# Kernel tuning notes

Hardware: AMD Instinct MI355X
Metric: run time of the kernel (lower is better)

Reference implementation:

```python
import jax, jax.numpy as jnp
import numpy as np

NEG = -1e9

def setup_inputs() -> dict:
    key = jax.random.key(0)
    k1, k2, k3, k4, k5 = jax.random.split(key, 5)
    B, S, D = 4, 2048, 1024
    x = jax.random.normal(k1, (B, S, D), dtype=jnp.float32)
    Wq = jax.random.normal(k2, (D, D), dtype=jnp.float32) * (1.0 / np.sqrt(D))
    Wk = jax.random.normal(k3, (D, D), dtype=jnp.float32) * (1.0 / np.sqrt(D))
    Wv = jax.random.normal(k4, (D, D), dtype=jnp.float32) * (1.0 / np.sqrt(D))
    mask = jax.random.randint(k5, (B, S), 0, 2) > 0  # bool [B,S]
    return {"x": x, "Wq": Wq, "Wk": Wk, "Wv": Wv, "mask": mask}

def reference(x, Wq, Wk, Wv, mask):
    # x: [B,S,D]; single-head self-attention, scale = 1/sqrt(D)
    D = x.shape[-1]
    scale = 1.0 / D ** 0.5
    q = jnp.einsum('bsi,ij->bsj', x, Wq)
    k = jnp.einsum('bsi,ij->bsj', x, Wk)
    y = jnp.einsum('bsi,bzi->bsz', q, k) * scale  # [B,S,S]
    # additive mask: (~mask)[:, :, None] * -1e9 broadcasts over key axis
    m = (~mask).astype(jnp.float32)[:, :, None]
    y = y + m * NEG
    v = jnp.einsum('bsi,ij->bsj', x, Wv)
    attn = jax.nn.softmax(y, axis=-1)
    return jnp.einsum('bsz,bzi->bsi', attn, v)
```

## Files before the change

kernel.cpp:

```cpp
#include <hip/hip_runtime.h>

typedef __bf16 bf16x8 __attribute__((ext_vector_type(8)));
typedef float f32x4 __attribute__((ext_vector_type(4)));
typedef unsigned short u16;

__device__ __forceinline__ u16 f2bf(float f) {
    union { float f; unsigned u; } v; v.f = f;
    unsigned r = (v.u + 0x7FFFu + ((v.u >> 16) & 1u)) >> 16;
    return (u16)r;
}

__device__ __forceinline__ void fence_bar() {
    asm volatile("" ::: "memory");
    __builtin_amdgcn_s_barrier();
    asm volatile("" ::: "memory");
}

__global__ __launch_bounds__(256)
void normMask(const unsigned int* __restrict__ m, unsigned char* __restrict__ nm) {
    __shared__ int isByte;
    if (threadIdx.x == 0) isByte = 0;
    __syncthreads();
    int bad = 0;
    for (int i = threadIdx.x; i < 2048; i += 256) bad |= (m[i] > 1u);
    if (bad) atomicOr(&isByte, 1);
    __syncthreads();
    if (isByte) {
        const unsigned char* mb = (const unsigned char*)m;
        for (int i = threadIdx.x; i < 8192; i += 256) nm[i] = mb[i] ? 1 : 0;
    } else {
        for (int i = threadIdx.x; i < 8192; i += 256) nm[i] = (unsigned char)m[i];
    }
}

__global__ __launch_bounds__(256)
void transW(const float* __restrict__ Wq, const float* __restrict__ Wk,
            const float* __restrict__ Wv, u16* __restrict__ Wt) {
    __shared__ u16 tile[64][65];
    const float* W = blockIdx.z == 0 ? Wq : (blockIdx.z == 1 ? Wk : Wv);
    u16* out = Wt + (size_t)blockIdx.z * 1024 * 1024;
    int k0 = blockIdx.x * 64, n0 = blockIdx.y * 64;
    int t = threadIdx.x, cl = t & 63, rw = t >> 6;
    #pragma unroll
    for (int r = 0; r < 16; ++r) {
        int row = r * 4 + rw;
        tile[cl][row] = f2bf(W[(size_t)(k0 + row) * 1024 + n0 + cl]);
    }
    __syncthreads();
    #pragma unroll
    for (int r = 0; r < 16; ++r) {
        int row = r * 4 + rw;
        out[(size_t)(n0 + row) * 1024 + k0 + cl] = tile[row][cl];
    }
}

__global__ __launch_bounds__(256)
void convX(const float* __restrict__ x, u16* __restrict__ xb) {
    const size_t n4 = (size_t)8192 * 1024 / 4;
    for (size_t i = (size_t)blockIdx.x * 256 + threadIdx.x; i < n4; i += (size_t)gridDim.x * 256) {
        float4 v = ((const float4*)x)[i];
        ushort4 o = make_ushort4(f2bf(v.x), f2bf(v.y), f2bf(v.z), f2bf(v.w));
        ((ushort4*)xb)[i] = o;
    }
}

__global__ __launch_bounds__(256)
void transV(const u16* __restrict__ qkv, u16* __restrict__ vt) {
    __shared__ u16 tile[64][65];
    int b = blockIdx.z;
    int s0 = blockIdx.x * 64, d0 = blockIdx.y * 64;
    int t = threadIdx.x, cl = t & 63, rw = t >> 6;
    const u16* src = qkv + (size_t)b * 2048 * 3072 + 2048;
    #pragma unroll
    for (int r = 0; r < 16; ++r) {
        int row = r * 4 + rw;
        tile[cl][row] = src[(size_t)(s0 + row) * 3072 + d0 + cl];
    }
    __syncthreads();
    u16* dst = vt + (size_t)b * 1024 * 2048;
    #pragma unroll
    for (int r = 0; r < 16; ++r) {
        int row = r * 4 + rw;
        dst[(size_t)(d0 + row) * 2048 + s0 + cl] = tile[row][cl];
    }
}

template <int OUTV>
__global__ __launch_bounds__(512, 2)
void gemm8p(const u16* __restrict__ A_, int lda, size_t sA,
            const u16* __restrict__ B_, int ldb, size_t sB,
            void* __restrict__ Cout, int ldc, size_t sC,
            int kdim, int ntiles) {
    __shared__ u16 lds[65536];
    const u16* A = A_ + (size_t)blockIdx.z * sA;
    const u16* B = B_ + (size_t)blockIdx.z * sB;

    const int bid = blockIdx.x;
    const int brow = (bid / ntiles) * 256, bcol = (bid % ntiles) * 256;
    const int t = threadIdx.x;
    const int w = t >> 6, l = t & 63;
    const int wr = w >> 2, wc = w & 3;

    const int srow = t >> 3;
    const int sslot = (t & 7) ^ (srow & 7);
    const int aBase = (wr * 128 + (l & 15)) * 64;
    const int bBase = 32768 + (wc * 64 + (l & 15)) * 64;
    const int cx0 = (((l >> 4)) ^ (l & 7)) * 8;
    const int cx1 = (((l >> 4) + 4) ^ (l & 7)) * 8;

    auto lds3 = (__attribute__((address_space(3))) char*)lds;

    #define ISSUE(matB, q, tt, buf) do {                                           \
        const u16* gsrc = ((matB) ? B : A)                                         \
            + (size_t)(((matB) ? bcol : brow) + (q) * 64 + srow) * ((matB) ? ldb : lda) \
            + (size_t)(tt) * 64 + sslot * 8;                                       \
        const int dst_ = ((matB) ? 32768 : 0) + (buf) * 16384 + (q) * 4096 + t * 8; \
        __builtin_amdgcn_global_load_lds(                                          \
            (const __attribute__((address_space(1))) void*)gsrc,                   \
            (__attribute__((address_space(3))) void*)(lds3 + 2 * dst_), 16, 0, 0); \
    } while (0)

    f32x4 acc[8][4];
    #pragma unroll
    for (int m = 0; m < 8; ++m)
        #pragma unroll
        for (int n = 0; n < 4; ++n)
            acc[m][n] = (f32x4){0.f, 0.f, 0.f, 0.f};

    const int NT = kdim >> 6;

    ISSUE(1, 0, 0, 0); ISSUE(1, 1, 0, 0); ISSUE(1, 2, 0, 0); ISSUE(1, 3, 0, 0);
    ISSUE(0, 0, 0, 0); ISSUE(0, 2, 0, 0); ISSUE(0, 1, 0, 0); ISSUE(0, 3, 0, 0);
    asm volatile("s_waitcnt vmcnt(2)" ::: "memory");
    fence_bar();

    for (int tt = 0; tt < NT; ++tt) {
        const int c = tt & 1;
        const int ab = c * 16384;
        const int nb = c ^ 1;
        const bool pf = (tt + 1 < NT);
        bf16x8 af[4], bfv[4];

        #pragma unroll
        for (int m = 0; m < 4; ++m) af[m] = *(const bf16x8*)&lds[ab + aBase + m * 1024 + cx0];
        #pragma unroll
        for (int n = 0; n < 4; ++n) bfv[n] = *(const bf16x8*)&lds[ab + bBase + n * 1024 + cx0];
        if (pf) {
            ISSUE(1, 0, tt + 1, nb); ISSUE(1, 1, tt + 1, nb);
            asm volatile("s_waitcnt vmcnt(2)" ::: "memory");
        } else {
            asm volatile("s_waitcnt vmcnt(0)" ::: "memory");
        }
        fence_bar();
        __builtin_amdgcn_s_setprio(1);
        #pragma unroll
        for (int m = 0; m < 4; ++m)
            #pragma unroll
            for (int n = 0; n < 4; ++n)
                acc[m][n] = __builtin_amdgcn_mfma_f32_16x16x32_bf16(af[m], bfv[n], acc[m][n], 0, 0, 0);
        __builtin_amdgcn_s_setprio(0);
        fence_bar();

        #pragma unroll
        for (int m = 0; m < 4; ++m) af[m] = *(const bf16x8*)&lds[ab + aBase + (m + 4) * 1024 + cx0];
        if (pf) { ISSUE(1, 2, tt + 1, nb); ISSUE(1, 3, tt + 1, nb); }
        fence_bar();
        __builtin_amdgcn_s_setprio(1);
        #pragma unroll
        for (int m = 0; m < 4; ++m)
            #pragma unroll
            for (int n = 0; n < 4; ++n)
                acc[m + 4][n] = __builtin_amdgcn_mfma_f32_16x16x32_bf16(af[m], bfv[n], acc[m + 4][n], 0, 0, 0);
        __builtin_amdgcn_s_setprio(0);
        fence_bar();

        #pragma unroll
        for (int m = 0; m < 4; ++m) af[m] = *(const bf16x8*)&lds[ab + aBase + m * 1024 + cx1];
        #pragma unroll
        for (int n = 0; n < 4; ++n) bfv[n] = *(const bf16x8*)&lds[ab + bBase + n * 1024 + cx1];
        if (pf) { ISSUE(0, 0, tt + 1, nb); ISSUE(0, 2, tt + 1, nb); }
        fence_bar();
        __builtin_amdgcn_s_setprio(1);
        #pragma unroll
        for (int m = 0; m < 4; ++m)
            #pragma unroll
            for (int n = 0; n < 4; ++n)
                acc[m][n] = __builtin_amdgcn_mfma_f32_16x16x32_bf16(af[m], bfv[n], acc[m][n], 0, 0, 0);
        __builtin_amdgcn_s_setprio(0);
        fence_bar();

        #pragma unroll
        for (int m = 0; m < 4; ++m) af[m] = *(const bf16x8*)&lds[ab + aBase + (m + 4) * 1024 + cx1];
        if (pf) {
            ISSUE(0, 1, tt + 1, nb); ISSUE(0, 3, tt + 1, nb);
            asm volatile("s_waitcnt vmcnt(2)" ::: "memory");
        } else {
            asm volatile("s_waitcnt vmcnt(0)" ::: "memory");
        }
        fence_bar();
        __builtin_amdgcn_s_setprio(1);
        #pragma unroll
        for (int m = 0; m < 4; ++m)
            #pragma unroll
            for (int n = 0; n < 4; ++n)
                acc[m + 4][n] = __builtin_amdgcn_mfma_f32_16x16x32_bf16(af[m], bfv[n], acc[m + 4][n], 0, 0, 0);
        __builtin_amdgcn_s_setprio(0);
        fence_bar();
    }
    #undef ISSUE

    const int lr = (l >> 4) * 4, lc = l & 15;
    #pragma unroll
    for (int m = 0; m < 8; ++m) {
        #pragma unroll
        for (int n = 0; n < 4; ++n) {
            int rr = brow + wr * 128 + m * 16 + lr;
            int cc = bcol + wc * 64 + n * 16 + lc;
            #pragma unroll
            for (int j = 0; j < 4; ++j) {
                if constexpr (OUTV == 0)
                    ((u16*)Cout)[(size_t)blockIdx.z * sC + (size_t)(rr + j) * ldc + cc] = f2bf(acc[m][n][j]);
                else
                    ((float*)Cout)[(size_t)blockIdx.z * sC + (size_t)(rr + j) * ldc + cc] = acc[m][n][j];
            }
        }
    }
}

template <int OUTV>
__global__ __launch_bounds__(256, 2)
void gemm_bt(const u16* __restrict__ A0, int lda, size_t sA,
             const u16* __restrict__ B0, int ldb, size_t sB,
             void* __restrict__ Cout, int ldc, size_t sC, int kdim) {
    __shared__ u16 lA[128 * 64];
    __shared__ u16 lB[128 * 64];
    const u16* A = A0 + (size_t)blockIdx.z * sA;
    const u16* B = B0 + (size_t)blockIdx.z * sB;
    const int t = threadIdx.x;
    const int w = t >> 6, l = t & 63;
    const int wr = w >> 1, wc = w & 1;
    const int brow = blockIdx.x * 128, bcol = blockIdx.y * 128;
    const int rt = l >> 3;
    const int cb = (l & 7) * 8;

    auto ldsA3 = (__attribute__((address_space(3))) char*)lA;
    auto ldsB3 = (__attribute__((address_space(3))) char*)lB;

    f32x4 acc[4][4];
    #pragma unroll
    for (int m = 0; m < 4; ++m)
        #pragma unroll
        for (int n = 0; n < 4; ++n)
            acc[m][n] = (f32x4){0.f, 0.f, 0.f, 0.f};

    for (int k0 = 0; k0 < kdim; k0 += 64) {
        __syncthreads();
        #pragma unroll
        for (int p = 0; p < 4; ++p) {
            int chunk = p * 4 + w;
            const u16* ga = A + (size_t)(brow + chunk * 8 + rt) * lda + k0 + cb;
            __builtin_amdgcn_global_load_lds(
                (const __attribute__((address_space(1))) void*)ga,
                (__attribute__((address_space(3))) void*)(ldsA3 + chunk * 1024), 16, 0, 0);
            const u16* gb = B + (size_t)(bcol + chunk * 8 + rt) * ldb + k0 + cb;
            __builtin_amdgcn_global_load_lds(
                (const __attribute__((address_space(1))) void*)gb,
                (__attribute__((address_space(3))) void*)(ldsB3 + chunk * 1024), 16, 0, 0);
        }
        __syncthreads();
        #pragma unroll
        for (int kk = 0; kk < 2; ++kk) {
            bf16x8 af[4], bfv[4];
            #pragma unroll
            for (int m = 0; m < 4; ++m)
                af[m] = *(const bf16x8*)&lA[(wr * 64 + m * 16 + (l & 15)) * 64 + kk * 32 + (l >> 4) * 8];
            #pragma unroll
            for (int n = 0; n < 4; ++n)
                bfv[n] = *(const bf16x8*)&lB[(wc * 64 + n * 16 + (l & 15)) * 64 + kk * 32 + (l >> 4) * 8];
            #pragma unroll
            for (int m = 0; m < 4; ++m)
                #pragma unroll
                for (int n = 0; n < 4; ++n)
                    acc[m][n] = __builtin_amdgcn_mfma_f32_16x16x32_bf16(af[m], bfv[n], acc[m][n], 0, 0, 0);
        }
    }

    const int lrow = (l >> 4) * 4, lcol = l & 15;
    #pragma unroll
    for (int m = 0; m < 4; ++m) {
        #pragma unroll
        for (int n = 0; n < 4; ++n) {
            int rr = brow + wr * 64 + m * 16 + lrow;
            int cc = bcol + wc * 64 + n * 16 + lcol;
            #pragma unroll
            for (int j = 0; j < 4; ++j) {
                if constexpr (OUTV == 0)
                    ((u16*)Cout)[(size_t)blockIdx.z * sC + (size_t)(rr + j) * ldc + cc] = f2bf(acc[m][n][j]);
                else
                    ((float*)Cout)[(size_t)blockIdx.z * sC + (size_t)(rr + j) * ldc + cc] = acc[m][n][j];
            }
        }
    }
}

__global__ __launch_bounds__(256)
void softmax_rows(const float* __restrict__ S0, size_t sS, u16* __restrict__ P0, size_t sP,
                  const unsigned char* __restrict__ nm, int bbase) {
    const int row = blockIdx.x, t = threadIdx.x;
    const int b = bbase + blockIdx.z;
    const float* S = S0 + (size_t)blockIdx.z * sS;
    u16* dst = P0 + (size_t)blockIdx.z * sP + (size_t)row * 2048;
    if (nm[b * 2048 + row] == 0) {
        ushort4 u = make_ushort4(0x3A00, 0x3A00, 0x3A00, 0x3A00);
        ((ushort4*)dst)[t] = u;
        ((ushort4*)dst)[t + 256] = u;
        return;
    }
    const float4* src = (const float4*)(S + (size_t)row * 2048);
    float4 a = src[t], c = src[t + 256];
    float v[8] = {a.x, a.y, a.z, a.w, c.x, c.y, c.z, c.w};
    float mx = -1e30f;
    #pragma unroll
    for (int i = 0; i < 8; ++i) { v[i] *= 0.03125f; mx = fmaxf(mx, v[i]); }
    #pragma unroll
    for (int o = 32; o > 0; o >>= 1) mx = fmaxf(mx, __shfl_xor(mx, o));
    __shared__ float redm[4], reds[4];
    if ((t & 63) == 0) redm[t >> 6] = mx;
    __syncthreads();
    mx = fmaxf(fmaxf(redm[0], redm[1]), fmaxf(redm[2], redm[3]));
    float s = 0.f;
    #pragma unroll
    for (int i = 0; i < 8; ++i) { v[i] = expf(v[i] - mx); s += v[i]; }
    #pragma unroll
    for (int o = 32; o > 0; o >>= 1) s += __shfl_xor(s, o);
    if ((t & 63) == 0) reds[t >> 6] = s;
    __syncthreads();
    s = (reds[0] + reds[1]) + (reds[2] + reds[3]);
    float inv = 1.0f / s;
    ushort4 o0 = make_ushort4(f2bf(v[0] * inv), f2bf(v[1] * inv), f2bf(v[2] * inv), f2bf(v[3] * inv));
    ushort4 o1 = make_ushort4(f2bf(v[4] * inv), f2bf(v[5] * inv), f2bf(v[6] * inv), f2bf(v[7] * inv));
    ((ushort4*)dst)[t] = o0;
    ((ushort4*)dst)[t + 256] = o1;
}

extern "C" void kernel_launch(void* const* d_in, const int* in_sizes, int n_in,
                              void* d_out, int out_size, void* d_ws, size_t ws_size,
                              hipStream_t stream) {
    const float* x  = (const float*)d_in[0];
    const float* Wq = (const float*)d_in[1];
    const float* Wk = (const float*)d_in[2];
    const float* Wv = (const float*)d_in[3];
    const unsigned int* mask = (const unsigned int*)d_in[4];
    float* out = (float*)d_out;

    char* p = (char*)d_ws;
    u16* Wt  = (u16*)p;  p += (size_t)3072 * 1024 * 2;
    u16* xb  = (u16*)p;  p += (size_t)8192 * 1024 * 2;
    u16* qkv = (u16*)p;  p += (size_t)8192 * 3072 * 2;
    u16* vt  = (u16*)p;  p += (size_t)4 * 1024 * 2048 * 2;
    char* base = p;
    const size_t sizeS = (size_t)2048 * 2048 * 4;
    const size_t sizeP = (size_t)2048 * 2048 * 2;
    bool batched = ws_size >= (size_t)(base - (char*)d_ws) + 4 * (sizeS + sizeP) + 8192;

    float* S = (float*)base;
    u16* P;
    unsigned char* nm;
    if (batched) {
        P  = (u16*)(base + 4 * sizeS);
        nm = (unsigned char*)(base + 4 * (sizeS + sizeP));
    } else {
        P  = (u16*)(base + sizeS);
        nm = (unsigned char*)(base + sizeS + sizeP);
    }

    normMask<<<1, 256, 0, stream>>>(mask, nm);
    transW<<<dim3(16, 16, 3), 256, 0, stream>>>(Wq, Wk, Wv, Wt);
    convX<<<2048, 256, 0, stream>>>(x, xb);
    gemm8p<0><<<dim3(384, 1, 1), 512, 0, stream>>>(
        xb, 1024, 0, Wt, 1024, 0, qkv, 3072, 0, 1024, 12);
    transV<<<dim3(32, 16, 4), 256, 0, stream>>>(qkv, vt);

    if (batched) {
        gemm8p<1><<<dim3(64, 1, 4), 512, 0, stream>>>(
            qkv, 3072, (size_t)2048 * 3072, qkv + 1024, 3072, (size_t)2048 * 3072,
            S, 2048, (size_t)2048 * 2048, 1024, 8);
        softmax_rows<<<dim3(2048, 1, 4), 256, 0, stream>>>(
            S, (size_t)2048 * 2048, P, (size_t)2048 * 2048, nm, 0);
        gemm_bt<2><<<dim3(16, 8, 4), 256, 0, stream>>>(
            P, 2048, (size_t)2048 * 2048, vt, 2048, (size_t)1024 * 2048,
            out, 1024, (size_t)2048 * 1024, 2048);
    } else {
        for (int b = 0; b < 4; ++b) {
            const u16* Qb = qkv + (size_t)b * 2048 * 3072;
            gemm8p<1><<<dim3(64, 1, 1), 512, 0, stream>>>(
                Qb, 3072, 0, Qb + 1024, 3072, 0, S, 2048, 0, 1024, 8);
            softmax_rows<<<dim3(2048, 1, 1), 256, 0, stream>>>(S, 0, P, 0, nm, b);
            gemm_bt<2><<<dim3(16, 8, 1), 256, 0, stream>>>(
                P, 2048, 0, vt + (size_t)b * 1024 * 2048, 2048, 0,
                out + (size_t)b * 2048 * 1024, 1024, 0, 2048);
        }
    }
}
```

Before: 201.3 us.

## Add XCD-aware block swizzle and issue whole next-tile prefetch at once

Adds a template flag that remaps block IDs so that consecutive tiles, which share A/B panels, land on the same XCD, aiming for better L2 reuse in the QKV projection and the batched QK^T GEMM. It also restructures the K-loop prefetch: instead of spreading the eight next-tile async loads across four compute stages, it waits for all outstanding loads and then issues all eight at the start of each iteration. The swizzle assumes the grid size divides by 8. The bulk prefetch trades finer-grained overlap for an earlier issue, and adds a full vmcnt(0) stall at the top of every iteration.

New measurement: 205.5 us. 2.1% more time.

```diff
diff --git a/kernel.cpp b/kernel.cpp
--- a/kernel.cpp
+++ b/kernel.cpp
@@ -85,7 +85,7 @@
     }
 }
 
-template <int OUTV>
+template <int OUTV, int SWZ>
 __global__ __launch_bounds__(512, 2)
 void gemm8p(const u16* __restrict__ A_, int lda, size_t sA,
             const u16* __restrict__ B_, int ldb, size_t sB,
@@ -95,7 +95,11 @@
     const u16* A = A_ + (size_t)blockIdx.z * sA;
     const u16* B = B_ + (size_t)blockIdx.z * sB;
 
-    const int bid = blockIdx.x;
+    int bid = blockIdx.x;
+    if (SWZ) {
+        int cpx = gridDim.x >> 3;
+        bid = (bid & 7) * cpx + (bid >> 3);
+    }
     const int brow = (bid / ntiles) * 256, bcol = (bid % ntiles) * 256;
     const int t = threadIdx.x;
     const int w = t >> 6, l = t & 63;
@@ -120,6 +124,13 @@
             (__attribute__((address_space(3))) void*)(lds3 + 2 * dst_), 16, 0, 0); \
     } while (0)
 
+    #define ISSUE8(tt, buf) do {                                                   \
+        ISSUE(1, 0, tt, buf); ISSUE(1, 1, tt, buf);                                \
+        ISSUE(1, 2, tt, buf); ISSUE(1, 3, tt, buf);                                \
+        ISSUE(0, 0, tt, buf); ISSUE(0, 2, tt, buf);                                \
+        ISSUE(0, 1, tt, buf); ISSUE(0, 3, tt, buf);                                \
+    } while (0)
+
     f32x4 acc[8][4];
     #pragma unroll
     for (int m = 0; m < 8; ++m)
@@ -129,9 +140,8 @@
 
     const int NT = kdim >> 6;
 
-    ISSUE(1, 0, 0, 0); ISSUE(1, 1, 0, 0); ISSUE(1, 2, 0, 0); ISSUE(1, 3, 0, 0);
-    ISSUE(0, 0, 0, 0); ISSUE(0, 2, 0, 0); ISSUE(0, 1, 0, 0); ISSUE(0, 3, 0, 0);
-    asm volatile("s_waitcnt vmcnt(2)" ::: "memory");
+    ISSUE8(0, 0);
+    asm volatile("s_waitcnt vmcnt(0)" ::: "memory");
     fence_bar();
 
     for (int tt = 0; tt < NT; ++tt) {
@@ -145,12 +155,8 @@
         for (int m = 0; m < 4; ++m) af[m] = *(const bf16x8*)&lds[ab + aBase + m * 1024 + cx0];
         #pragma unroll
         for (int n = 0; n < 4; ++n) bfv[n] = *(const bf16x8*)&lds[ab + bBase + n * 1024 + cx0];
-        if (pf) {
-            ISSUE(1, 0, tt + 1, nb); ISSUE(1, 1, tt + 1, nb);
-            asm volatile("s_waitcnt vmcnt(2)" ::: "memory");
-        } else {
-            asm volatile("s_waitcnt vmcnt(0)" ::: "memory");
-        }
+        asm volatile("s_waitcnt vmcnt(0)" ::: "memory");
+        if (pf) ISSUE8(tt + 1, nb);
         fence_bar();
         __builtin_amdgcn_s_setprio(1);
         #pragma unroll
@@ -163,7 +169,6 @@
 
         #pragma unroll
         for (int m = 0; m < 4; ++m) af[m] = *(const bf16x8*)&lds[ab + aBase + (m + 4) * 1024 + cx0];
-        if (pf) { ISSUE(1, 2, tt + 1, nb); ISSUE(1, 3, tt + 1, nb); }
         fence_bar();
         __builtin_amdgcn_s_setprio(1);
         #pragma unroll
@@ -178,7 +183,6 @@
         for (int m = 0; m < 4; ++m) af[m] = *(const bf16x8*)&lds[ab + aBase + m * 1024 + cx1];
         #pragma unroll
         for (int n = 0; n < 4; ++n) bfv[n] = *(const bf16x8*)&lds[ab + bBase + n * 1024 + cx1];
-        if (pf) { ISSUE(0, 0, tt + 1, nb); ISSUE(0, 2, tt + 1, nb); }
         fence_bar();
         __builtin_amdgcn_s_setprio(1);
         #pragma unroll
@@ -191,12 +195,8 @@
 
         #pragma unroll
         for (int m = 0; m < 4; ++m) af[m] = *(const bf16x8*)&lds[ab + aBase + (m + 4) * 1024 + cx1];
-        if (pf) {
-            ISSUE(0, 1, tt + 1, nb); ISSUE(0, 3, tt + 1, nb);
-            asm volatile("s_waitcnt vmcnt(2)" ::: "memory");
-        } else {
-            asm volatile("s_waitcnt vmcnt(0)" ::: "memory");
-        }
+        if (pf) asm volatile("s_waitcnt vmcnt(2)" ::: "memory");
+        else    asm volatile("s_waitcnt vmcnt(0)" ::: "memory");
         fence_bar();
         __builtin_amdgcn_s_setprio(1);
         #pragma unroll
@@ -207,6 +207,7 @@
         __builtin_amdgcn_s_setprio(0);
         fence_bar();
     }
+    #undef ISSUE8
     #undef ISSUE
 
     const int lr = (l >> 4) * 4, lc = l & 15;
@@ -377,12 +378,12 @@
     normMask<<<1, 256, 0, stream>>>(mask, nm);
     transW<<<dim3(16, 16, 3), 256, 0, stream>>>(Wq, Wk, Wv, Wt);
     convX<<<2048, 256, 0, stream>>>(x, xb);
-    gemm8p<0><<<dim3(384, 1, 1), 512, 0, stream>>>(
+    gemm8p<0, 1><<<dim3(384, 1, 1), 512, 0, stream>>>(
         xb, 1024, 0, Wt, 1024, 0, qkv, 3072, 0, 1024, 12);
     transV<<<dim3(32, 16, 4), 256, 0, stream>>>(qkv, vt);
 
     if (batched) {
-        gemm8p<1><<<dim3(64, 1, 4), 512, 0, stream>>>(
+        gemm8p<1, 1><<<dim3(64, 1, 4), 512, 0, stream>>>(
             qkv, 3072, (size_t)2048 * 3072, qkv + 1024, 3072, (size_t)2048 * 3072,
             S, 2048, (size_t)2048 * 2048, 1024, 8);
         softmax_rows<<<dim3(2048, 1, 4), 256, 0, stream>>>(
@@ -393,7 +394,7 @@
     } else {
         for (int b = 0; b < 4; ++b) {
             const u16* Qb = qkv + (size_t)b * 2048 * 3072;
-            gemm8p<1><<<dim3(64, 1, 1), 512, 0, stream>>>(
+            gemm8p<1, 0><<<dim3(64, 1, 1), 512, 0, stream>>>(
                 Qb, 3072, 0, Qb + 1024, 3072, 0, S, 2048, 0, 1024, 8);
             softmax_rows<<<dim3(2048, 1, 1), 256, 0, stream>>>(S, 0, P, 0, nm, b);
             gemm_bt<2><<<dim3(16, 8, 1), 256, 0, stream>>>(
```

## Fuse softmax into QK epilogue stats and PV GEMM prologue

Applied to the files above, without the earlier changes.

Drops the separate softmax kernel and the bf16 P matrix. The QK^T GEMM epilogue now writes per-row partial max and sum-exp for each 64-column slice, a small kernel combines these into a row max and inverse sum, and the PV GEMM recomputes exp from the fp32 scores as it loads them into shared memory. The 1/sqrt(D) scale is folded into Wq during its bf16 conversion, and masked rows are encoded as a negative inverse-sum sentinel that yields a uniform 1/2048. The aim is to skip one full read of S and a write plus read of P, at the cost of exp work and register-path fp32 loads inside the PV GEMM's load loop in place of async global-to-LDS copies.

After: 256.6 us. 27.5% more time.

```diff
diff --git a/kernel.cpp b/kernel.cpp
--- a/kernel.cpp
+++ b/kernel.cpp
@@ -38,13 +38,14 @@
             const float* __restrict__ Wv, u16* __restrict__ Wt) {
     __shared__ u16 tile[64][65];
     const float* W = blockIdx.z == 0 ? Wq : (blockIdx.z == 1 ? Wk : Wv);
+    const float sc = blockIdx.z == 0 ? 0.03125f : 1.0f;
     u16* out = Wt + (size_t)blockIdx.z * 1024 * 1024;
     int k0 = blockIdx.x * 64, n0 = blockIdx.y * 64;
     int t = threadIdx.x, cl = t & 63, rw = t >> 6;
     #pragma unroll
     for (int r = 0; r < 16; ++r) {
         int row = r * 4 + rw;
-        tile[cl][row] = f2bf(W[(size_t)(k0 + row) * 1024 + n0 + cl]);
+        tile[cl][row] = f2bf(W[(size_t)(k0 + row) * 1024 + n0 + cl] * sc);
     }
     __syncthreads();
     #pragma unroll
@@ -90,7 +91,7 @@
 void gemm8p(const u16* __restrict__ A_, int lda, size_t sA,
             const u16* __restrict__ B_, int ldb, size_t sB,
             void* __restrict__ Cout, int ldc, size_t sC,
-            int kdim, int ntiles) {
+            int kdim, int ntiles, float2* __restrict__ partPtr) {
     __shared__ u16 lds[65536];
     const u16* A = A_ + (size_t)blockIdx.z * sA;
     const u16* B = B_ + (size_t)blockIdx.z * sB;
@@ -225,16 +226,61 @@
             }
         }
     }
-}
-
-template <int OUTV>
+    if constexpr (OUTV == 1) {
+        float2* part = partPtr + ((size_t)blockIdx.z * 32 + (bcol >> 6) + wc) * 2048;
+        #pragma unroll
+        for (int m = 0; m < 8; ++m) {
+            #pragma unroll
+            for (int j = 0; j < 4; ++j) {
+                float mx = fmaxf(fmaxf(acc[m][0][j], acc[m][1][j]),
+                                 fmaxf(acc[m][2][j], acc[m][3][j]));
+                #pragma unroll
+                for (int o = 1; o < 16; o <<= 1) mx = fmaxf(mx, __shfl_xor(mx, o));
+                float se = 0.f;
+                #pragma unroll
+                for (int n = 0; n < 4; ++n) se += __expf(acc[m][n][j] - mx);
+                #pragma unroll
+                for (int o = 1; o < 16; o <<= 1) se += __shfl_xor(se, o);
+                if ((l & 15) == 0) {
+                    int rr = brow + wr * 128 + m * 16 + (l >> 4) * 4 + j;
+                    part[rr] = make_float2(mx, se);
+                }
+            }
+        }
+    }
+}
+
+__global__ __launch_bounds__(256)
+void combineStats(const float2* __restrict__ part, float2* __restrict__ stats,
+                  const unsigned char* __restrict__ nm, int bbase) {
+    const int row = blockIdx.x * 256 + threadIdx.x;
+    const int z = blockIdx.y;
+    if (nm[(bbase + z) * 2048 + row] == 0) {
+        stats[z * 2048 + row] = make_float2(0.f, -(1.0f / 2048.0f));
+        return;
+    }
+    const float2* p = part + (size_t)z * 32 * 2048 + row;
+    float m = -1e30f;
+    #pragma unroll
+    for (int c = 0; c < 32; ++c) m = fmaxf(m, p[(size_t)c * 2048].x);
+    float Z = 0.f;
+    #pragma unroll
+    for (int c = 0; c < 32; ++c) {
+        float2 v = p[(size_t)c * 2048];
+        Z += v.y * __expf(v.x - m);
+    }
+    stats[z * 2048 + row] = make_float2(m, 1.0f / Z);
+}
+
 __global__ __launch_bounds__(256, 2)
-void gemm_bt(const u16* __restrict__ A0, int lda, size_t sA,
+void gemm_pv(const float* __restrict__ S0, size_t sS,
+             const float2* __restrict__ st0,
              const u16* __restrict__ B0, int ldb, size_t sB,
-             void* __restrict__ Cout, int ldc, size_t sC, int kdim) {
+             float* __restrict__ Cout, int ldc, size_t sC, int kdim) {
     __shared__ u16 lA[128 * 64];
     __shared__ u16 lB[128 * 64];
-    const u16* A = A0 + (size_t)blockIdx.z * sA;
+    const float* S = S0 + (size_t)blockIdx.z * sS;
+    const float2* st = st0 + (size_t)blockIdx.z * 2048;
     const u16* B = B0 + (size_t)blockIdx.z * sB;
     const int t = threadIdx.x;
     const int w = t >> 6, l = t & 63;
@@ -243,8 +289,14 @@
     const int rt = l >> 3;
     const int cb = (l & 7) * 8;
 
-    auto ldsA3 = (__attribute__((address_space(3))) char*)lA;
     auto ldsB3 = (__attribute__((address_space(3))) char*)lB;
+
+    float sm[4], siz[4];
+    #pragma unroll
+    for (int p = 0; p < 4; ++p) {
+        float2 v = st[brow + (p * 4 + w) * 8 + rt];
+        sm[p] = v.x; siz[p] = v.y;
+    }
 
     f32x4 acc[4][4];
     #pragma unroll
@@ -258,14 +310,22 @@
         #pragma unroll
         for (int p = 0; p < 4; ++p) {
             int chunk = p * 4 + w;
-            const u16* ga = A + (size_t)(brow + chunk * 8 + rt) * lda + k0 + cb;
-            __builtin_amdgcn_global_load_lds(
-                (const __attribute__((address_space(1))) void*)ga,
-                (__attribute__((address_space(3))) void*)(ldsA3 + chunk * 1024), 16, 0, 0);
             const u16* gb = B + (size_t)(bcol + chunk * 8 + rt) * ldb + k0 + cb;
             __builtin_amdgcn_global_load_lds(
                 (const __attribute__((address_space(1))) void*)gb,
                 (__attribute__((address_space(3))) void*)(ldsB3 + chunk * 1024), 16, 0, 0);
+            const float4* sp = (const float4*)(S + (size_t)(brow + chunk * 8 + rt) * 2048 + k0 + cb);
+            float4 a0 = sp[0], a1 = sp[1];
+            float m = sm[p], iz = siz[p];
+            float pv[8] = {a0.x, a0.y, a0.z, a0.w, a1.x, a1.y, a1.z, a1.w};
+            unsigned ou[4];
+            #pragma unroll
+            for (int i = 0; i < 4; ++i) {
+                float p0 = iz < 0.f ? -iz : __expf(pv[2 * i]     - m) * iz;
+                float p1 = iz < 0.f ? -iz : __expf(pv[2 * i + 1] - m) * iz;
+                ou[i] = (unsigned)f2bf(p0) | ((unsigned)f2bf(p1) << 16);
+            }
+            *(uint4*)&lA[chunk * 512 + l * 8] = make_uint4(ou[0], ou[1], ou[2], ou[3]);
         }
         __syncthreads();
         #pragma unroll
@@ -293,54 +353,10 @@
             int rr = brow + wr * 64 + m * 16 + lrow;
             int cc = bcol + wc * 64 + n * 16 + lcol;
             #pragma unroll
-            for (int j = 0; j < 4; ++j) {
-                if constexpr (OUTV == 0)
-                    ((u16*)Cout)[(size_t)blockIdx.z * sC + (size_t)(rr + j) * ldc + cc] = f2bf(acc[m][n][j]);
-                else
-                    ((float*)Cout)[(size_t)blockIdx.z * sC + (size_t)(rr + j) * ldc + cc] = acc[m][n][j];
-            }
-        }
-    }
-}
-
-__global__ __launch_bounds__(256)
-void softmax_rows(const float* __restrict__ S0, size_t sS, u16* __restrict__ P0, size_t sP,
-                  const unsigned char* __restrict__ nm, int bbase) {
-    const int row = blockIdx.x, t = threadIdx.x;
-    const int b = bbase + blockIdx.z;
-    const float* S = S0 + (size_t)blockIdx.z * sS;
-    u16* dst = P0 + (size_t)blockIdx.z * sP + (size_t)row * 2048;
-    if (nm[b * 2048 + row] == 0) {
-        ushort4 u = make_ushort4(0x3A00, 0x3A00, 0x3A00, 0x3A00);
-        ((ushort4*)dst)[t] = u;
-        ((ushort4*)dst)[t + 256] = u;
-        return;
-    }
-    const float4* src = (const float4*)(S + (size_t)row * 2048);
-    float4 a = src[t], c = src[t + 256];
-    float v[8] = {a.x, a.y, a.z, a.w, c.x, c.y, c.z, c.w};
-    float mx = -1e30f;
-    #pragma unroll
-    for (int i = 0; i < 8; ++i) { v[i] *= 0.03125f; mx = fmaxf(mx, v[i]); }
-    #pragma unroll
-    for (int o = 32; o > 0; o >>= 1) mx = fmaxf(mx, __shfl_xor(mx, o));
-    __shared__ float redm[4], reds[4];
-    if ((t & 63) == 0) redm[t >> 6] = mx;
-    __syncthreads();
-    mx = fmaxf(fmaxf(redm[0], redm[1]), fmaxf(redm[2], redm[3]));
-    float s = 0.f;
-    #pragma unroll
-    for (int i = 0; i < 8; ++i) { v[i] = expf(v[i] - mx); s += v[i]; }
-    #pragma unroll
-    for (int o = 32; o > 0; o >>= 1) s += __shfl_xor(s, o);
-    if ((t & 63) == 0) reds[t >> 6] = s;
-    __syncthreads();
-    s = (reds[0] + reds[1]) + (reds[2] + reds[3]);
-    float inv = 1.0f / s;
-    ushort4 o0 = make_ushort4(f2bf(v[0] * inv), f2bf(v[1] * inv), f2bf(v[2] * inv), f2bf(v[3] * inv));
-    ushort4 o1 = make_ushort4(f2bf(v[4] * inv), f2bf(v[5] * inv), f2bf(v[6] * inv), f2bf(v[7] * inv));
-    ((ushort4*)dst)[t] = o0;
-    ((ushort4*)dst)[t + 256] = o1;
+            for (int j = 0; j < 4; ++j)
+                Cout[(size_t)blockIdx.z * sC + (size_t)(rr + j) * ldc + cc] = acc[m][n][j];
+        }
+    }
 }
 
 extern "C" void kernel_launch(void* const* d_in, const int* in_sizes, int n_in,
@@ -359,45 +375,41 @@
     u16* qkv = (u16*)p;  p += (size_t)8192 * 3072 * 2;
     u16* vt  = (u16*)p;  p += (size_t)4 * 1024 * 2048 * 2;
     char* base = p;
-    const size_t sizeS = (size_t)2048 * 2048 * 4;
-    const size_t sizeP = (size_t)2048 * 2048 * 2;
-    bool batched = ws_size >= (size_t)(base - (char*)d_ws) + 4 * (sizeS + sizeP) + 8192;
-
-    float* S = (float*)base;
-    u16* P;
-    unsigned char* nm;
-    if (batched) {
-        P  = (u16*)(base + 4 * sizeS);
-        nm = (unsigned char*)(base + 4 * (sizeS + sizeP));
-    } else {
-        P  = (u16*)(base + sizeS);
-        nm = (unsigned char*)(base + sizeS + sizeP);
-    }
+    const size_t sizeS  = (size_t)2048 * 2048 * 4;
+    const size_t sizePt = (size_t)32 * 2048 * 8;
+    const size_t sizeSt = (size_t)2048 * 8;
+    bool batched = ws_size >= (size_t)(base - (char*)d_ws) + 4 * (sizeS + sizePt + sizeSt) + 8192;
+
+    float* S; float2* part; float2* stats; unsigned char* nm;
+    int nz = batched ? 4 : 1;
+    S     = (float*)base;
+    part  = (float2*)(base + nz * sizeS);
+    stats = (float2*)(base + nz * (sizeS + sizePt));
+    nm    = (unsigned char*)(base + nz * (sizeS + sizePt + sizeSt));
 
     normMask<<<1, 256, 0, stream>>>(mask, nm);
     transW<<<dim3(16, 16, 3), 256, 0, stream>>>(Wq, Wk, Wv, Wt);
     convX<<<2048, 256, 0, stream>>>(x, xb);
     gemm8p<0><<<dim3(384, 1, 1), 512, 0, stream>>>(
-        xb, 1024, 0, Wt, 1024, 0, qkv, 3072, 0, 1024, 12);
+        xb, 1024, 0, Wt, 1024, 0, qkv, 3072, 0, 1024, 12, nullptr);
     transV<<<dim3(32, 16, 4), 256, 0, stream>>>(qkv, vt);
 
     if (batched) {
         gemm8p<1><<<dim3(64, 1, 4), 512, 0, stream>>>(
             qkv, 3072, (size_t)2048 * 3072, qkv + 1024, 3072, (size_t)2048 * 3072,
-            S, 2048, (size_t)2048 * 2048, 1024, 8);
-        softmax_rows<<<dim3(2048, 1, 4), 256, 0, stream>>>(
-            S, (size_t)2048 * 2048, P, (size_t)2048 * 2048, nm, 0);
-        gemm_bt<2><<<dim3(16, 8, 4), 256, 0, stream>>>(
-            P, 2048, (size_t)2048 * 2048, vt, 2048, (size_t)1024 * 2048,
+            S, 2048, (size_t)2048 * 2048, 1024, 8, part);
+        combineStats<<<dim3(8, 4), 256, 0, stream>>>(part, stats, nm, 0);
+        gemm_pv<<<dim3(16, 8, 4), 256, 0, stream>>>(
+            S, (size_t)2048 * 2048, stats, vt, 2048, (size_t)1024 * 2048,
             out, 1024, (size_t)2048 * 1024, 2048);
     } else {
         for (int b = 0; b < 4; ++b) {
             const u16* Qb = qkv + (size_t)b * 2048 * 3072;
             gemm8p<1><<<dim3(64, 1, 1), 512, 0, stream>>>(
-                Qb, 3072, 0, Qb + 1024, 3072, 0, S, 2048, 0, 1024, 8);
-            softmax_rows<<<dim3(2048, 1, 1), 256, 0, stream>>>(S, 0, P, 0, nm, b);
-            gemm_bt<2><<<dim3(16, 8, 1), 256, 0, stream>>>(
-                P, 2048, 0, vt + (size_t)b * 1024 * 2048, 2048, 0,
+                Qb, 3072, 0, Qb + 1024, 3072, 0, S, 2048, 0, 1024, 8, part);
+            combineStats<<<dim3(8, 1), 256, 0, stream>>>(part, stats, nm, b);
+            gemm_pv<<<dim3(16, 8, 1), 256, 0, stream>>>(
+                S, 0, stats, vt + (size_t)b * 1024 * 2048, 2048, 0,
                 out + (size_t)b * 2048 * 1024, 1024, 0, 2048);
         }
     }
```

## Replace LDS-staged attention GEMMs with register-direct global loads and double buffering

Applied to the files above, without the earlier changes.

Swaps the LDS-staged gemm_bt and the persistent gemm8p for the QK^T and PV products with a new gemm_reg kernel. Each lane loads its MFMA fragments straight from global memory into registers, double-buffered over 32-wide k steps, with no shared memory and no barriers. This drops LDS traffic and sync overhead but gives up reuse across waves, so each tile is reloaded from global/L2 several times and more memory bandwidth is needed. The occupancy hint of 2 in launch_bounds is also removed.

After: 343.6 us (median of 4 runs). +70.7%, slower.

```diff
diff --git a/kernel.cpp b/kernel.cpp
--- a/kernel.cpp
+++ b/kernel.cpp
@@ -228,23 +228,25 @@
 }
 
 template <int OUTV>
-__global__ __launch_bounds__(256, 2)
-void gemm_bt(const u16* __restrict__ A0, int lda, size_t sA,
-             const u16* __restrict__ B0, int ldb, size_t sB,
-             void* __restrict__ Cout, int ldc, size_t sC, int kdim) {
-    __shared__ u16 lA[128 * 64];
-    __shared__ u16 lB[128 * 64];
+__global__ __launch_bounds__(256)
+void gemm_reg(const u16* __restrict__ A0, int lda, size_t sA,
+              const u16* __restrict__ B0, int ldb, size_t sB,
+              float* __restrict__ Cout, int ldc, size_t sC, int kdim) {
     const u16* A = A0 + (size_t)blockIdx.z * sA;
     const u16* B = B0 + (size_t)blockIdx.z * sB;
     const int t = threadIdx.x;
     const int w = t >> 6, l = t & 63;
     const int wr = w >> 1, wc = w & 1;
     const int brow = blockIdx.x * 128, bcol = blockIdx.y * 128;
-    const int rt = l >> 3;
-    const int cb = (l & 7) * 8;
-
-    auto ldsA3 = (__attribute__((address_space(3))) char*)lA;
-    auto ldsB3 = (__attribute__((address_space(3))) char*)lB;
+
+    const u16* pA[4];
+    const u16* pB[4];
+    #pragma unroll
+    for (int m = 0; m < 4; ++m)
+        pA[m] = A + (size_t)(brow + wr * 64 + m * 16 + (l & 15)) * lda + (l >> 4) * 8;
+    #pragma unroll
+    for (int n = 0; n < 4; ++n)
+        pB[n] = B + (size_t)(bcol + wc * 64 + n * 16 + (l & 15)) * ldb + (l >> 4) * 8;
 
     f32x4 acc[4][4];
     #pragma unroll
@@ -253,37 +255,34 @@
         for (int n = 0; n < 4; ++n)
             acc[m][n] = (f32x4){0.f, 0.f, 0.f, 0.f};
 
-    for (int k0 = 0; k0 < kdim; k0 += 64) {
-        __syncthreads();
-        #pragma unroll
-        for (int p = 0; p < 4; ++p) {
-            int chunk = p * 4 + w;
-            const u16* ga = A + (size_t)(brow + chunk * 8 + rt) * lda + k0 + cb;
-            __builtin_amdgcn_global_load_lds(
-                (const __attribute__((address_space(1))) void*)ga,
-                (__attribute__((address_space(3))) void*)(ldsA3 + chunk * 1024), 16, 0, 0);
-            const u16* gb = B + (size_t)(bcol + chunk * 8 + rt) * ldb + k0 + cb;
-            __builtin_amdgcn_global_load_lds(
-                (const __attribute__((address_space(1))) void*)gb,
-                (__attribute__((address_space(3))) void*)(ldsB3 + chunk * 1024), 16, 0, 0);
-        }
-        __syncthreads();
-        #pragma unroll
-        for (int kk = 0; kk < 2; ++kk) {
-            bf16x8 af[4], bfv[4];
-            #pragma unroll
-            for (int m = 0; m < 4; ++m)
-                af[m] = *(const bf16x8*)&lA[(wr * 64 + m * 16 + (l & 15)) * 64 + kk * 32 + (l >> 4) * 8];
-            #pragma unroll
-            for (int n = 0; n < 4; ++n)
-                bfv[n] = *(const bf16x8*)&lB[(wc * 64 + n * 16 + (l & 15)) * 64 + kk * 32 + (l >> 4) * 8];
-            #pragma unroll
-            for (int m = 0; m < 4; ++m)
-                #pragma unroll
-                for (int n = 0; n < 4; ++n)
-                    acc[m][n] = __builtin_amdgcn_mfma_f32_16x16x32_bf16(af[m], bfv[n], acc[m][n], 0, 0, 0);
-        }
-    }
+    #define LOADH(aa, bb, h) do {                                        \
+        const int ko = (h) * 32;                                         \
+        _Pragma("unroll")                                                \
+        for (int m = 0; m < 4; ++m) aa[m] = *(const bf16x8*)(pA[m] + ko);\
+        _Pragma("unroll")                                                \
+        for (int n = 0; n < 4; ++n) bb[n] = *(const bf16x8*)(pB[n] + ko);\
+    } while (0)
+
+    #define MFMA16(aa, bb) do {                                          \
+        _Pragma("unroll")                                                \
+        for (int m = 0; m < 4; ++m)                                      \
+            _Pragma("unroll")                                            \
+            for (int n = 0; n < 4; ++n)                                  \
+                acc[m][n] = __builtin_amdgcn_mfma_f32_16x16x32_bf16(     \
+                    aa[m], bb[n], acc[m][n], 0, 0, 0);                   \
+    } while (0)
+
+    const int NH = kdim >> 5;
+    bf16x8 a0[4], b0[4], a1[4], b1[4];
+    LOADH(a0, b0, 0);
+    for (int h = 0; h < NH; h += 2) {
+        if (h + 1 < NH) LOADH(a1, b1, h + 1);
+        MFMA16(a0, b0);
+        if (h + 2 < NH) LOADH(a0, b0, h + 2);
+        if (h + 1 < NH) MFMA16(a1, b1);
+    }
+    #undef LOADH
+    #undef MFMA16
 
     const int lrow = (l >> 4) * 4, lcol = l & 15;
     #pragma unroll
@@ -293,12 +292,8 @@
             int rr = brow + wr * 64 + m * 16 + lrow;
             int cc = bcol + wc * 64 + n * 16 + lcol;
             #pragma unroll
-            for (int j = 0; j < 4; ++j) {
-                if constexpr (OUTV == 0)
-                    ((u16*)Cout)[(size_t)blockIdx.z * sC + (size_t)(rr + j) * ldc + cc] = f2bf(acc[m][n][j]);
-                else
-                    ((float*)Cout)[(size_t)blockIdx.z * sC + (size_t)(rr + j) * ldc + cc] = acc[m][n][j];
-            }
+            for (int j = 0; j < 4; ++j)
+                Cout[(size_t)blockIdx.z * sC + (size_t)(rr + j) * ldc + cc] = acc[m][n][j];
         }
     }
 }
@@ -382,21 +377,21 @@
     transV<<<dim3(32, 16, 4), 256, 0, stream>>>(qkv, vt);
 
     if (batched) {
-        gemm8p<1><<<dim3(64, 1, 4), 512, 0, stream>>>(
+        gemm_reg<1><<<dim3(16, 16, 4), 256, 0, stream>>>(
             qkv, 3072, (size_t)2048 * 3072, qkv + 1024, 3072, (size_t)2048 * 3072,
-            S, 2048, (size_t)2048 * 2048, 1024, 8);
+            S, 2048, (size_t)2048 * 2048, 1024);
         softmax_rows<<<dim3(2048, 1, 4), 256, 0, stream>>>(
             S, (size_t)2048 * 2048, P, (size_t)2048 * 2048, nm, 0);
-        gemm_bt<2><<<dim3(16, 8, 4), 256, 0, stream>>>(
+        gemm_reg<2><<<dim3(16, 8, 4), 256, 0, stream>>>(
             P, 2048, (size_t)2048 * 2048, vt, 2048, (size_t)1024 * 2048,
             out, 1024, (size_t)2048 * 1024, 2048);
     } else {
         for (int b = 0; b < 4; ++b) {
             const u16* Qb = qkv + (size_t)b * 2048 * 3072;
-            gemm8p<1><<<dim3(64, 1, 1), 512, 0, stream>>>(
-                Qb, 3072, 0, Qb + 1024, 3072, 0, S, 2048, 0, 1024, 8);
+            gemm_reg<1><<<dim3(16, 16, 1), 256, 0, stream>>>(
+                Qb, 3072, 0, Qb + 1024, 3072, 0, S, 2048, 0, 1024);
             softmax_rows<<<dim3(2048, 1, 1), 256, 0, stream>>>(S, 0, P, 0, nm, b);
-            gemm_bt<2><<<dim3(16, 8, 1), 256, 0, stream>>>(
+            gemm_reg<2><<<dim3(16, 8, 1), 256, 0, stream>>>(
                 P, 2048, 0, vt + (size_t)b * 1024 * 2048, 2048, 0,
                 out + (size_t)b * 2048 * 1024, 1024, 0, 2048);
         }
```
